# Optimization experiments

Hardware: AMD Instinct MI355X
Metric: run time of the kernel (lower is better)

Reference implementation:

```python
import jax, jax.numpy as jnp
import numpy as np

B, C_IN, C_OUT, H, W = 8, 256, 256, 48, 48


def setup_inputs() -> dict:
    key = jax.random.key(0)
    ks = jax.random.split(key, 8)
    s = 1.0 / np.sqrt(C_IN)
    return {
        "x1": jax.random.normal(ks[0], (B, C_IN, H, W), dtype=jnp.float32),
        "x2": jax.random.normal(ks[1], (B, C_IN, H, W), dtype=jnp.float32),
        "Wq": jax.random.normal(ks[2], (C_OUT, C_IN), dtype=jnp.float32) * s,
        "bq": jax.random.normal(ks[3], (C_OUT,), dtype=jnp.float32) * s,
        "Wk": jax.random.normal(ks[4], (C_OUT, C_IN), dtype=jnp.float32) * s,
        "bk": jax.random.normal(ks[5], (C_OUT,), dtype=jnp.float32) * s,
        "Wv": jax.random.normal(ks[6], (C_OUT, C_IN), dtype=jnp.float32) * s,
        "bv": jax.random.normal(ks[7], (C_OUT,), dtype=jnp.float32) * s,
    }


def _conv1x1(x, Wt, b):
    # x: [B,Cin,H,W], Wt: [Cout,Cin] -> [B,Cout,H,W]
    return jnp.einsum("bchw,oc->bohw", x, Wt) + b[None, :, None, None]


def reference(x1, x2, Wq, bq, Wk, bk, Wv, bv):
    q = _conv1x1(x1, Wq, bq)  # [B,C,H,W]
    k = _conv1x1(x2, Wk, bk)
    v = _conv1x1(x2, Wv, bv)
    b, c, h, w = q.shape
    n = h * w
    qf = q.reshape(b, c, n).transpose(0, 2, 1)  # [B,N,C]
    kf = k.reshape(b, c, n)                      # [B,C,N]
    vf = v.reshape(b, c, n).transpose(0, 2, 1)   # [B,N,C]
    # NOTE: faithful to source -- no 1/sqrt(d) scaling, no head split
    attn = jax.nn.softmax(jnp.einsum("bic,bcj->bij", qf, kf), axis=-1)  # [B,N,N]
    out = jnp.einsum("bij,bjc->bic", attn, vf)   # [B,N,C]
    return out.transpose(0, 2, 1).reshape(b, c, h, w)
```

## Files before the change

kernel.cpp:

```cpp
#include <hip/hip_runtime.h>
#include <cfloat>
#include <cstddef>
#include <cstdint>

#define BATCH 8
#define CDIM  256
#define NTOK  2304

typedef float    f32x4  __attribute__((ext_vector_type(4)));
typedef float    f32x16 __attribute__((ext_vector_type(16)));
typedef _Float16 f16x8  __attribute__((ext_vector_type(8)));
typedef _Float16 f16x4  __attribute__((ext_vector_type(4)));

#define MFMA16(a, b, c) __builtin_amdgcn_mfma_f32_16x16x32_f16(a, b, c, 0, 0, 0)
#define MFMA32(a, b, c) __builtin_amdgcn_mfma_f32_32x32x16_f16(a, b, c, 0, 0, 0)

__device__ __forceinline__ void gl_lds16(const void* g, void* l) {
    __builtin_amdgcn_global_load_lds(
        (const __attribute__((address_space(1))) void*)g,
        (__attribute__((address_space(3))) void*)l, 16, 0, 0);
}

__global__ __launch_bounds__(256) void cast_fused(
    const float* __restrict__ x1, const float* __restrict__ x2,
    const float* __restrict__ Wq, const float* __restrict__ Wk,
    const float* __restrict__ Wv,
    _Float16* __restrict__ Xt1, _Float16* __restrict__ Xt2,
    _Float16* __restrict__ Wh)
{
    const int tid = threadIdx.x;
    int bx = blockIdx.x;

    if (bx < 192) {
        int i = (bx * 256 + tid) * 4;
        const float* src = (i < 65536) ? (Wq + i)
                         : (i < 131072) ? (Wk + (i - 65536)) : (Wv + (i - 131072));
        float4 v = *(const float4*)src;
        f16x4 h = { (_Float16)v.x, (_Float16)v.y, (_Float16)v.z, (_Float16)v.w };
        *(f16x4*)(Wh + i) = h;
        return;
    }
    bx -= 192;
    const int n0 = (bx % 36) * 64;
    const int rest = bx / 36;
    const int c0 = (rest & 3) * 64;
    const int bz = rest >> 2;
    const float* X   = (bz < 8) ? x1 : x2;
    _Float16*   Xt   = (bz < 8) ? Xt1 : Xt2;
    const int b = bz & 7;

    __shared__ _Float16 T[64][72];

    {
        const int cl = tid >> 2, nch = (tid & 3) * 16;
        const float* src = X + (size_t)(b * CDIM + c0 + cl) * NTOK + n0 + nch;
#pragma unroll
        for (int u = 0; u < 4; ++u) {
            float4 v = *(const float4*)(src + u * 4);
            T[cl][nch + u * 4 + 0] = (_Float16)v.x;
            T[cl][nch + u * 4 + 1] = (_Float16)v.y;
            T[cl][nch + u * 4 + 2] = (_Float16)v.z;
            T[cl][nch + u * 4 + 3] = (_Float16)v.w;
        }
    }
    __syncthreads();
    {
        const int nl = tid >> 2, cch = (tid & 3) * 16;
        _Float16* dst = Xt + (size_t)(b * NTOK + n0 + nl) * CDIM + c0 + cch;
        f16x8 o0, o1;
#pragma unroll
        for (int i = 0; i < 8; ++i) {
            o0[i] = T[cch + i][nl];
            o1[i] = T[cch + 8 + i][nl];
        }
        *(f16x8*)dst = o0;
        *(f16x8*)(dst + 8) = o1;
    }
}

__global__ __launch_bounds__(256, 2) void proj_mfma(
    const _Float16* __restrict__ Xt1, const _Float16* __restrict__ Xt2,
    const _Float16* __restrict__ Wh,
    const float* __restrict__ bq, const float* __restrict__ bk,
    const float* __restrict__ bv,
    _Float16* __restrict__ Qo, _Float16* __restrict__ Ko, _Float16* __restrict__ Vo)
{
    const int tid  = threadIdx.x;
    const int lane = tid & 63;
    const int w    = tid >> 6;
    const int l15  = lane & 15, l4 = lane >> 4;
    const int n0   = blockIdx.x * 64;
    const int mode = blockIdx.y;
    const int b    = blockIdx.z;

    const _Float16* Xt = (mode == 0) ? Xt1 : Xt2;
    const _Float16* Wm = Wh + mode * 65536;
    const float* bias  = (mode == 0) ? bq : (mode == 1) ? bk : bv;
    _Float16* OUT      = (mode == 0) ? Qo : (mode == 1) ? Ko : Vo;

    __shared__ __align__(16) char sm[65536];
    _Float16* Xl = (_Float16*)sm;
    _Float16* Wl = (_Float16*)(sm + 32768);

#pragma unroll
    for (int t = 0; t < 8; ++t) {
        int i = w * 8 + t;
        int row = 2 * i + (lane >> 5);
        int ch  = lane & 31;
        gl_lds16(Xt + (size_t)(b * NTOK + n0 + row) * CDIM + ((ch ^ (row & 7)) * 8),
                 (char*)Xl + i * 1024);
    }

    float bias_o[4];
#pragma unroll
    for (int ot = 0; ot < 4; ++ot) bias_o[ot] = bias[w * 64 + ot * 16 + l15];

    f32x4 acc[16];
#pragma unroll
    for (int i = 0; i < 16; ++i) acc[i] = (f32x4){0.f, 0.f, 0.f, 0.f};

    for (int c0 = 0; c0 < CDIM; c0 += 64) {
        __syncthreads();
#pragma unroll
        for (int t = 0; t < 8; ++t) {
            int i = w * 8 + t;
            int row = 8 * i + (lane >> 3);
            int ch  = lane & 7;
            gl_lds16(Wm + (size_t)row * CDIM + c0 + ((ch ^ (row & 7)) * 8),
                     (char*)Wl + i * 1024);
        }
        __syncthreads();

#pragma unroll
        for (int kk2 = 0; kk2 < 2; ++kk2) {
            f16x8 a[4], bf[4];
#pragma unroll
            for (int nt = 0; nt < 4; ++nt) {
                int row = nt * 16 + l15;
                int ch  = ((c0 >> 3) + kk2 * 4 + l4) ^ (row & 7);
                a[nt] = *(const f16x8*)((const char*)Xl + row * 512 + ch * 16);
            }
#pragma unroll
            for (int ot = 0; ot < 4; ++ot) {
                int row = w * 64 + ot * 16 + l15;
                int ch  = (kk2 * 4 + l4) ^ (row & 7);
                bf[ot] = *(const f16x8*)((const char*)Wl + row * 128 + ch * 16);
            }
#pragma unroll
            for (int nt = 0; nt < 4; ++nt)
#pragma unroll
                for (int ot = 0; ot < 4; ++ot)
                    acc[nt * 4 + ot] = MFMA16(a[nt], bf[ot], acc[nt * 4 + ot]);
        }
    }

    __syncthreads();

    if (mode <= 1) {
        _Float16* Dl = (_Float16*)sm;
#pragma unroll
        for (int nt = 0; nt < 4; ++nt)
#pragma unroll
            for (int ot = 0; ot < 4; ++ot)
#pragma unroll
                for (int reg = 0; reg < 4; ++reg)
                    Dl[(nt * 16 + 4 * l4 + reg) * 256 + w * 64 + ot * 16 + l15] =
                        (_Float16)(acc[nt * 4 + ot][reg] + bias_o[ot]);
        __syncthreads();
        char* dst = (char*)(OUT + ((size_t)b * NTOK + n0) * CDIM);
#pragma unroll
        for (int u = 0; u < 8; ++u) {
            f16x8 v = *(const f16x8*)((const char*)Dl + u * 4096 + tid * 16);
            *(f16x8*)(dst + u * 4096 + tid * 16) = v;
        }
    } else {
        _Float16* Dlv = (_Float16*)sm;
#pragma unroll
        for (int nt = 0; nt < 4; ++nt)
#pragma unroll
            for (int ot = 0; ot < 4; ++ot)
#pragma unroll
                for (int reg = 0; reg < 4; ++reg)
                    Dlv[(w * 64 + ot * 16 + l15) * 80 + nt * 16 + 4 * l4 + reg] =
                        (_Float16)(acc[nt * 4 + ot][reg] + bias_o[ot]);
        __syncthreads();
#pragma unroll
        for (int t = 0; t < 8; ++t) {
            int ro = (w * 8 + t) * 8 + (lane >> 3);
            f16x8 v = *(const f16x8*)((const char*)Dlv + ro * 160 + (lane & 7) * 16);
            *(f16x8*)(OUT + ((size_t)b * CDIM + ro) * NTOK + n0 + (lane & 7) * 8) = v;
        }
    }
}

template <int SEG>
__global__ __launch_bounds__(512, 2) void attn_fa(
    const _Float16* __restrict__ Q, const _Float16* __restrict__ K,
    const _Float16* __restrict__ Vt, _Float16* __restrict__ pacc,
    float2* __restrict__ pml)
{
    const int tid  = threadIdx.x;
    const int lane = tid & 63;
    const int w    = tid >> 6;
    const int l31  = lane & 31;
    const int h    = lane >> 5;

    const int nb  = 9 * BATCH * SEG, cpx = nb / 8;
    const int bid = blockIdx.x;
    const int swz = (bid & 7) * cpx + (bid >> 3);
    const int x = swz % 9;
    const int b = (swz / 9) & 7;
    const int z = swz / 72;

    const int row0   = x * 256 + w * 32;
    const int jbase  = z * (NTOK / SEG);
    const int NTILES = NTOK / SEG / 64;

    __shared__ __align__(16) char smem[131072];

    const _Float16* kSrc0; const _Float16* kSrc1;
    const _Float16* kSrc2; const _Float16* kSrc3;
    const _Float16* vSrc0; const _Float16* vSrc1;
    const _Float16* vSrc2; const _Float16* vSrc3;
    {
        const size_t kbb = (size_t)b * NTOK;
        const size_t vbb = (size_t)b * CDIM * NTOK;
        const int chunk = lane & 31;
        const int vch   = lane & 7;
        const int vr    = lane >> 3;
#pragma unroll
        for (int t = 0; t < 4; ++t) {
            int i  = w * 4 + t;
            int lr = 2 * i + h;
            int gr = (lr & 51) | ((lr & 4) << 1) | ((lr & 8) >> 1);
            const _Float16* ks =
                K + (kbb + jbase + gr) * CDIM + ((chunk ^ (lr & 7)) * 8);
            int vrow = 8 * i + vr;
            const _Float16* vs =
                Vt + vbb + (size_t)vrow * NTOK + jbase + ((vch ^ (vrow & 7)) * 8);
            if (t == 0) { kSrc0 = ks; vSrc0 = vs; }
            else if (t == 1) { kSrc1 = ks; vSrc1 = vs; }
            else if (t == 2) { kSrc2 = ks; vSrc2 = vs; }
            else { kSrc3 = ks; vSrc3 = vs; }
        }
    }

    f16x8 qa[16];
    {
        const _Float16* qb = Q + ((size_t)b * NTOK + row0 + l31) * CDIM + h * 8;
#pragma unroll
        for (int kk = 0; kk < 16; ++kk)
            qa[kk] = __builtin_nontemporal_load((const f16x8*)(qb + kk * 16));
    }

    f32x16 acc[8];
#pragma unroll
    for (int cb = 0; cb < 8; ++cb)
#pragma unroll
        for (int e = 0; e < 16; ++e) acc[cb][e] = 0.f;
    float m  = -FLT_MAX;
    float ps = 0.f;

    const int ldsDstK = w * 4096;
    const int ldsDstV = 32768 + w * 4096;

    auto stage = [&](int buf) {
        char* base = smem + buf * 65536;
        gl_lds16(kSrc0, base + ldsDstK);
        gl_lds16(kSrc1, base + ldsDstK + 1024);
        gl_lds16(kSrc2, base + ldsDstK + 2048);
        gl_lds16(kSrc3, base + ldsDstK + 3072);
        gl_lds16(vSrc0, base + ldsDstV);
        gl_lds16(vSrc1, base + ldsDstV + 1024);
        gl_lds16(vSrc2, base + ldsDstV + 2048);
        gl_lds16(vSrc3, base + ldsDstV + 3072);
        kSrc0 += 64 * CDIM; kSrc1 += 64 * CDIM;
        kSrc2 += 64 * CDIM; kSrc3 += 64 * CDIM;
        vSrc0 += 64; vSrc1 += 64; vSrc2 += 64; vSrc3 += 64;
    };

    stage(0);
    __syncthreads();

    const int xs = l31 & 7;

    for (int jt = 0; jt < NTILES; ++jt) {
        const int cur = jt & 1;

        if (jt + 1 < NTILES) stage(cur ^ 1);

        const char* Klc = (const char*)smem + cur * 65536;
        const char* Vlc = Klc + 32768;

#pragma unroll 1
        for (int jb = 0; jb < 2; ++jb) {
            f32x16 s;
#pragma unroll
            for (int e = 0; e < 16; ++e) s[e] = 0.f;
            const char* kb = Klc + (jb * 32 + l31) * 512;
#pragma unroll
            for (int kk = 0; kk < 16; ++kk) {
                f16x8 kf = *(const f16x8*)(kb + (((kk * 2 + h) ^ xs) * 16));
                s = MFMA32(kf, qa[kk], s);
            }

            float pm = s[0];
#pragma unroll
            for (int e = 1; e < 16; ++e) pm = fmaxf(pm, s[e]);
            pm = fmaxf(pm, __shfl_xor(pm, 32));
            if (pm > m + 8.f) {
                float sc = __expf(m - pm);
                m = pm;
                ps *= sc;
#pragma unroll
                for (int cb = 0; cb < 8; ++cb)
#pragma unroll
                    for (int e = 0; e < 16; ++e) acc[cb][e] *= sc;
            }

            f16x8 pa0, pa1;
#pragma unroll
            for (int e = 0; e < 8; ++e) {
                float p0 = __expf(s[e] - m);
                float p1 = __expf(s[8 + e] - m);
                ps += p0 + p1;
                pa0[e] = (_Float16)p0;
                pa1[e] = (_Float16)p1;
            }

            const int o0 = ((jb * 4 + 0 + h) ^ xs) * 16;
            const int o1 = ((jb * 4 + 2 + h) ^ xs) * 16;
#pragma unroll
            for (int cb = 0; cb < 8; ++cb) {
                const char* vb0 = Vlc + (cb * 32 + l31) * 128;
                f16x8 v0 = *(const f16x8*)(vb0 + o0);
                acc[cb] = MFMA32(v0, pa0, acc[cb]);
                f16x8 v1 = *(const f16x8*)(vb0 + o1);
                acc[cb] = MFMA32(v1, pa1, acc[cb]);
            }
        }

        __syncthreads();
    }

    float l_full = ps + __shfl_xor(ps, 32);
    float inv = 1.f / l_full;
    const size_t pbase = ((size_t)z * BATCH + b) * NTOK * CDIM;
    _Float16* stg = (_Float16*)(smem + w * 8448);

#pragma unroll
    for (int pass = 0; pass < 2; ++pass) {
#pragma unroll
        for (int cb4 = 0; cb4 < 4; ++cb4) {
            const f32x16 a = acc[pass * 4 + cb4];
#pragma unroll
            for (int g = 0; g < 4; ++g) {
                f16x4 o = { (_Float16)(a[4 * g + 0] * inv),
                            (_Float16)(a[4 * g + 1] * inv),
                            (_Float16)(a[4 * g + 2] * inv),
                            (_Float16)(a[4 * g + 3] * inv) };
                *(f16x4*)&stg[l31 * 132 + cb4 * 32 + g * 8 + h * 4] = o;
            }
        }
        asm volatile("s_waitcnt lgkmcnt(0)" ::: "memory");
        __builtin_amdgcn_sched_barrier(0);
        {
            char* dst = (char*)(pacc + pbase + (size_t)row0 * CDIM) + pass * 256;
#pragma unroll
            for (int u = 0; u < 8; ++u) {
                int r = u * 4 + (lane >> 4);
                f16x8 v = *(const f16x8*)((const char*)stg + r * 264 + (lane & 15) * 16);
                *(f16x8*)(dst + (size_t)r * 512 + (lane & 15) * 16) = v;
            }
        }
        asm volatile("s_waitcnt lgkmcnt(0)" ::: "memory");
        __builtin_amdgcn_sched_barrier(0);
    }
    if (lane < 32)
        pml[((size_t)z * BATCH + b) * NTOK + row0 + lane] = make_float2(m, l_full);
}

template <int SEG>
__global__ __launch_bounds__(256) void merge_kernel(
    const _Float16* __restrict__ pacc, const float2* __restrict__ pml,
    float* __restrict__ out)
{
    const int tid = threadIdx.x;
    const int n0 = blockIdx.x * 64;
    const int cc = blockIdx.y;
    const int b  = blockIdx.z;

    __shared__ float wgt[SEG][64];
    __shared__ float dinv[64];
    __shared__ float T[64][68];

    if (tid < 64) {
        int n = n0 + tid;
        float ms[SEG], ls[SEG];
#pragma unroll
        for (int s = 0; s < SEG; ++s) {
            float2 v = pml[((size_t)s * BATCH + b) * NTOK + n];
            ms[s] = v.x; ls[s] = v.y;
        }
        float M = ms[0];
#pragma unroll
        for (int s = 1; s < SEG; ++s) M = fmaxf(M, ms[s]);
        float den = 0.f;
#pragma unroll
        for (int s = 0; s < SEG; ++s) {
            float g = ls[s] * __expf(ms[s] - M);
            wgt[s][tid] = g;
            den += g;
        }
        dinv[tid] = 1.f / den;
    }
    __syncthreads();

    {
        const int nl = tid >> 2, cg = (tid & 3) * 16;
        float a[16];
#pragma unroll
        for (int u = 0; u < 16; ++u) a[u] = 0.f;
#pragma unroll
        for (int s = 0; s < SEG; ++s) {
            const _Float16* p = pacc + (((size_t)s * BATCH + b) * NTOK + n0 + nl) * CDIM
                                + cc * 64 + cg;
            f16x8 v0 = ((const f16x8*)p)[0];
            f16x8 v1 = ((const f16x8*)p)[1];
            float g = wgt[s][nl];
#pragma unroll
            for (int u = 0; u < 8; ++u) {
                a[u]     += g * (float)v0[u];
                a[8 + u] += g * (float)v1[u];
            }
        }
        float di = dinv[nl];
#pragma unroll
        for (int u = 0; u < 16; ++u) T[nl][cg + u] = a[u] * di;
    }
    __syncthreads();
    {
        const int cl = tid >> 2, nb2 = (tid & 3) * 16;
        float* ob = out + ((size_t)b * CDIM + cc * 64 + cl) * NTOK + n0 + nb2;
#pragma unroll
        for (int u = 0; u < 4; ++u) {
            float4 v = { T[nb2 + u * 4 + 0][cl], T[nb2 + u * 4 + 1][cl],
                         T[nb2 + u * 4 + 2][cl], T[nb2 + u * 4 + 3][cl] };
            *(float4*)&ob[u * 4] = v;
        }
    }
}

extern "C" void kernel_launch(void* const* d_in, const int* in_sizes, int n_in,
                              void* d_out, int out_size, void* d_ws, size_t ws_size,
                              hipStream_t stream)
{
    const float* x1 = (const float*)d_in[0];
    const float* x2 = (const float*)d_in[1];
    const float* Wq = (const float*)d_in[2];
    const float* bq = (const float*)d_in[3];
    const float* Wk = (const float*)d_in[4];
    const float* bk = (const float*)d_in[5];
    const float* Wv = (const float*)d_in[6];
    const float* bv = (const float*)d_in[7];
    float* out = (float*)d_out;

    const size_t plane = (size_t)BATCH * NTOK * CDIM;
    _Float16* ws16 = (_Float16*)d_ws;
    _Float16* Q   = ws16;
    _Float16* K   = ws16 + plane;
    _Float16* Vt  = ws16 + 2 * plane;
    _Float16* Xt1 = ws16 + 3 * plane;
    _Float16* Xt2 = ws16 + 4 * plane;
    _Float16* Wh  = ws16 + 5 * plane;
    const size_t fixed16 = 5 * plane + 196608;

    auto need = [&](size_t S) {
        return fixed16 * 2 + S * plane * 2 + S * (size_t)BATCH * NTOK * 8;
    };
    const int SEG = (ws_size >= need(3)) ? 3 : (ws_size >= need(2)) ? 2 : 1;

    _Float16* pacc = ws16 + fixed16;
    float2*   pml  = (float2*)((char*)d_ws + fixed16 * 2 + (size_t)SEG * plane * 2);

    cast_fused<<<dim3(192 + 36 * 4 * 16), dim3(256), 0, stream>>>(
        x1, x2, Wq, Wk, Wv, Xt1, Xt2, Wh);
    proj_mfma<<<dim3(36, 3, BATCH), dim3(256), 0, stream>>>(
        Xt1, Xt2, Wh, bq, bk, bv, Q, K, Vt);

    const int nb = 9 * BATCH;
    if (SEG == 3) {
        attn_fa<3><<<dim3(nb * 3), dim3(512), 0, stream>>>(Q, K, Vt, pacc, pml);
        merge_kernel<3><<<dim3(36, 4, BATCH), dim3(256), 0, stream>>>(pacc, pml, out);
    } else if (SEG == 2) {
        attn_fa<2><<<dim3(nb * 2), dim3(512), 0, stream>>>(Q, K, Vt, pacc, pml);
        merge_kernel<2><<<dim3(36, 4, BATCH), dim3(256), 0, stream>>>(pacc, pml, out);
    } else {
        attn_fa<1><<<dim3(nb), dim3(512), 0, stream>>>(Q, K, Vt, pacc, pml);
        merge_kernel<1><<<dim3(36, 4, BATCH), dim3(256), 0, stream>>>(pacc, pml, out);
    }
}
```

Before: 114.8 us.

## Fuse input cast/transpose into projection kernel and use nontemporal merge I/O

Removes the separate pass that casts x1/x2 to fp16 and transposes them into a workspace. Instead, each projection block loads fp32 input tiles per channel chunk, converts them, and transposes through an extra LDS buffer into the swizzled layout. This saves writing and re-reading the transposed fp16 copies, but x2 is now read and cast twice (for K and V), and each chunk needs extra barriers and about 9 KB more LDS, which may lower occupancy. The merge kernel also switches to nontemporal loads and stores.

```diff
diff --git a/kernel.cpp b/kernel.cpp
--- a/kernel.cpp
+++ b/kernel.cpp
@@ -21,65 +21,20 @@
         (__attribute__((address_space(3))) void*)l, 16, 0, 0);
 }
 
-__global__ __launch_bounds__(256) void cast_fused(
+__global__ __launch_bounds__(256) void cast_w(
+    const float* __restrict__ Wq, const float* __restrict__ Wk,
+    const float* __restrict__ Wv, _Float16* __restrict__ Wh)
+{
+    int i = (blockIdx.x * 256 + threadIdx.x) * 4;
+    const float* src = (i < 65536) ? (Wq + i)
+                     : (i < 131072) ? (Wk + (i - 65536)) : (Wv + (i - 131072));
+    float4 v = *(const float4*)src;
+    f16x4 h = { (_Float16)v.x, (_Float16)v.y, (_Float16)v.z, (_Float16)v.w };
+    *(f16x4*)(Wh + i) = h;
+}
+
+__global__ __launch_bounds__(256, 2) void proj_mfma(
     const float* __restrict__ x1, const float* __restrict__ x2,
-    const float* __restrict__ Wq, const float* __restrict__ Wk,
-    const float* __restrict__ Wv,
-    _Float16* __restrict__ Xt1, _Float16* __restrict__ Xt2,
-    _Float16* __restrict__ Wh)
-{
-    const int tid = threadIdx.x;
-    int bx = blockIdx.x;
-
-    if (bx < 192) {
-        int i = (bx * 256 + tid) * 4;
-        const float* src = (i < 65536) ? (Wq + i)
-                         : (i < 131072) ? (Wk + (i - 65536)) : (Wv + (i - 131072));
-        float4 v = *(const float4*)src;
-        f16x4 h = { (_Float16)v.x, (_Float16)v.y, (_Float16)v.z, (_Float16)v.w };
-        *(f16x4*)(Wh + i) = h;
-        return;
-    }
-    bx -= 192;
-    const int n0 = (bx % 36) * 64;
-    const int rest = bx / 36;
-    const int c0 = (rest & 3) * 64;
-    const int bz = rest >> 2;
-    const float* X   = (bz < 8) ? x1 : x2;
-    _Float16*   Xt   = (bz < 8) ? Xt1 : Xt2;
-    const int b = bz & 7;
-
-    __shared__ _Float16 T[64][72];
-
-    {
-        const int cl = tid >> 2, nch = (tid & 3) * 16;
-        const float* src = X + (size_t)(b * CDIM + c0 + cl) * NTOK + n0 + nch;
-#pragma unroll
-        for (int u = 0; u < 4; ++u) {
-            float4 v = *(const float4*)(src + u * 4);
-            T[cl][nch + u * 4 + 0] = (_Float16)v.x;
-            T[cl][nch + u * 4 + 1] = (_Float16)v.y;
-            T[cl][nch + u * 4 + 2] = (_Float16)v.z;
-            T[cl][nch + u * 4 + 3] = (_Float16)v.w;
-        }
-    }
-    __syncthreads();
-    {
-        const int nl = tid >> 2, cch = (tid & 3) * 16;
-        _Float16* dst = Xt + (size_t)(b * NTOK + n0 + nl) * CDIM + c0 + cch;
-        f16x8 o0, o1;
-#pragma unroll
-        for (int i = 0; i < 8; ++i) {
-            o0[i] = T[cch + i][nl];
-            o1[i] = T[cch + 8 + i][nl];
-        }
-        *(f16x8*)dst = o0;
-        *(f16x8*)(dst + 8) = o1;
-    }
-}
-
-__global__ __launch_bounds__(256, 2) void proj_mfma(
-    const _Float16* __restrict__ Xt1, const _Float16* __restrict__ Xt2,
     const _Float16* __restrict__ Wh,
     const float* __restrict__ bq, const float* __restrict__ bk,
     const float* __restrict__ bv,
@@ -93,23 +48,15 @@
     const int mode = blockIdx.y;
     const int b    = blockIdx.z;
 
-    const _Float16* Xt = (mode == 0) ? Xt1 : Xt2;
+    const float* X     = (mode == 0) ? x1 : x2;
     const _Float16* Wm = Wh + mode * 65536;
     const float* bias  = (mode == 0) ? bq : (mode == 1) ? bk : bv;
     _Float16* OUT      = (mode == 0) ? Qo : (mode == 1) ? Ko : Vo;
 
-    __shared__ __align__(16) char sm[65536];
-    _Float16* Xl = (_Float16*)sm;
-    _Float16* Wl = (_Float16*)(sm + 32768);
-
-#pragma unroll
-    for (int t = 0; t < 8; ++t) {
-        int i = w * 8 + t;
-        int row = 2 * i + (lane >> 5);
-        int ch  = lane & 31;
-        gl_lds16(Xt + (size_t)(b * NTOK + n0 + row) * CDIM + ((ch ^ (row & 7)) * 8),
-                 (char*)Xl + i * 1024);
-    }
+    __shared__ __align__(16) char sm[74752];
+    _Float16* Xl  = (_Float16*)sm;
+    _Float16* Wl  = (_Float16*)(sm + 32768);
+    _Float16* T16 = (_Float16*)(sm + 65536);
 
     float bias_o[4];
 #pragma unroll
@@ -121,6 +68,7 @@
 
     for (int c0 = 0; c0 < CDIM; c0 += 64) {
         __syncthreads();
+
 #pragma unroll
         for (int t = 0; t < 8; ++t) {
             int i = w * 8 + t;
@@ -128,6 +76,38 @@
             int ch  = lane & 7;
             gl_lds16(Wm + (size_t)row * CDIM + c0 + ((ch ^ (row & 7)) * 8),
                      (char*)Wl + i * 1024);
+        }
+
+        {
+            const int cl = tid >> 2, ngb = (tid & 3) * 16;
+            const float* src = X + (size_t)(b * CDIM + c0 + cl) * NTOK + n0 + ngb;
+            f16x8 h0, h1;
+#pragma unroll
+            for (int u = 0; u < 2; ++u) {
+                float4 va = *(const float4*)(src + u * 8);
+                float4 vb = *(const float4*)(src + u * 8 + 4);
+                f16x8& h = u ? h1 : h0;
+                h[0] = (_Float16)va.x; h[1] = (_Float16)va.y;
+                h[2] = (_Float16)va.z; h[3] = (_Float16)va.w;
+                h[4] = (_Float16)vb.x; h[5] = (_Float16)vb.y;
+                h[6] = (_Float16)vb.z; h[7] = (_Float16)vb.w;
+            }
+            *(f16x8*)&T16[cl * 72 + ngb]     = h0;
+            *(f16x8*)&T16[cl * 72 + ngb + 8] = h1;
+        }
+        __syncthreads();
+
+        {
+            const int nl = tid >> 2, cgb = (tid & 3) * 16;
+            f16x8 o0, o1;
+#pragma unroll
+            for (int i = 0; i < 8; ++i) {
+                o0[i] = T16[(cgb + i) * 72 + nl];
+                o1[i] = T16[(cgb + 8 + i) * 72 + nl];
+            }
+            const int ch0 = (c0 + cgb) >> 3;
+            *(f16x8*)((char*)Xl + nl * 512 + ((ch0 ^ (nl & 7)) * 16))       = o0;
+            *(f16x8*)((char*)Xl + nl * 512 + (((ch0 + 1) ^ (nl & 7)) * 16)) = o1;
         }
         __syncthreads();
 
@@ -425,8 +405,8 @@
         for (int s = 0; s < SEG; ++s) {
             const _Float16* p = pacc + (((size_t)s * BATCH + b) * NTOK + n0 + nl) * CDIM
                                 + cc * 64 + cg;
-            f16x8 v0 = ((const f16x8*)p)[0];
-            f16x8 v1 = ((const f16x8*)p)[1];
+            f16x8 v0 = __builtin_nontemporal_load((const f16x8*)p);
+            f16x8 v1 = __builtin_nontemporal_load(((const f16x8*)p) + 1);
             float g = wgt[s][nl];
 #pragma unroll
             for (int u = 0; u < 8; ++u) {
@@ -444,9 +424,9 @@
         float* ob = out + ((size_t)b * CDIM + cc * 64 + cl) * NTOK + n0 + nb2;
 #pragma unroll
         for (int u = 0; u < 4; ++u) {
-            float4 v = { T[nb2 + u * 4 + 0][cl], T[nb2 + u * 4 + 1][cl],
-                         T[nb2 + u * 4 + 2][cl], T[nb2 + u * 4 + 3][cl] };
-            *(float4*)&ob[u * 4] = v;
+            f32x4 v = { T[nb2 + u * 4 + 0][cl], T[nb2 + u * 4 + 1][cl],
+                        T[nb2 + u * 4 + 2][cl], T[nb2 + u * 4 + 3][cl] };
+            __builtin_nontemporal_store(v, (f32x4*)&ob[u * 4]);
         }
     }
 }
@@ -470,10 +450,8 @@
     _Float16* Q   = ws16;
     _Float16* K   = ws16 + plane;
     _Float16* Vt  = ws16 + 2 * plane;
-    _Float16* Xt1 = ws16 + 3 * plane;
-    _Float16* Xt2 = ws16 + 4 * plane;
-    _Float16* Wh  = ws16 + 5 * plane;
-    const size_t fixed16 = 5 * plane + 196608;
+    _Float16* Wh  = ws16 + 3 * plane;
+    const size_t fixed16 = 3 * plane + 196608;
 
     auto need = [&](size_t S) {
         return fixed16 * 2 + S * plane * 2 + S * (size_t)BATCH * NTOK * 8;
@@ -483,10 +461,9 @@
     _Float16* pacc = ws16 + fixed16;
     float2*   pml  = (float2*)((char*)d_ws + fixed16 * 2 + (size_t)SEG * plane * 2);
 
-    cast_fused<<<dim3(192 + 36 * 4 * 16), dim3(256), 0, stream>>>(
-        x1, x2, Wq, Wk, Wv, Xt1, Xt2, Wh);
+    cast_w<<<dim3(192), dim3(256), 0, stream>>>(Wq, Wk, Wv, Wh);
     proj_mfma<<<dim3(36, 3, BATCH), dim3(256), 0, stream>>>(
-        Xt1, Xt2, Wh, bq, bk, bv, Q, K, Vt);
+        x1, x2, Wh, bq, bk, bv, Q, K, Vt);
 
     const int nb = 9 * BATCH;
     if (SEG == 3) {
```

New measurement: 132.1 us. 15.1% more time.
